# Performance work log

Measured on AMD Instinct MI355X. Metric: run time of the kernel, lower is better.

The kernel has to match this reference:

```python
import jax, jax.numpy as jnp
import numpy as np

B, S, D, H = 64, 512, 512, 512


def setup_inputs() -> dict:
    key = jax.random.key(0)
    ks = jax.random.split(key, 8)
    k = 1.0 / np.sqrt(H)  # torch nn.LSTM init bound
    return {
        "x": jax.random.normal(ks[0], (B, S, D), dtype=jnp.float32),
        "emb": jax.random.normal(ks[1], (B, D), dtype=jnp.float32),
        "h_n": jax.random.normal(ks[2], (1, B, H), dtype=jnp.float32),
        "c_n": jax.random.normal(ks[3], (1, B, H), dtype=jnp.float32),
        "W_ih": jax.random.uniform(ks[4], (4 * H, D), jnp.float32, -k, k),
        "W_hh": jax.random.uniform(ks[5], (4 * H, H), jnp.float32, -k, k),
        "b_ih": jax.random.uniform(ks[6], (4 * H,), jnp.float32, -k, k),
        "b_hh": jax.random.uniform(ks[7], (4 * H,), jnp.float32, -k, k),
    }


def reference(x, emb, h_n, c_n, W_ih, W_hh, b_ih, b_hh):
    # Decoder feeds emb at step 0, then teacher-forces x[:, i-1] at step i.
    inputs = jnp.concatenate([emb[:, None, :], x[:, :-1, :]], axis=1)  # [B,S,D]
    # Precompute input-to-hidden gates for the whole sequence (one big GEMM).
    xg = jnp.einsum("bsd,gd->bsg", inputs, W_ih) + b_ih + b_hh  # [B,S,4H]

    def step(carry, xg_t):
        h, c = carry
        gates = xg_t + h @ W_hh.T  # [B,4H]; torch gate order: i,f,g,o
        i, f, g, o = jnp.split(gates, 4, axis=-1)
        c = jax.nn.sigmoid(f) * c + jax.nn.sigmoid(i) * jnp.tanh(g)
        h = jax.nn.sigmoid(o) * jnp.tanh(c)
        return (h, c), h

    (_, _), ys = jax.lax.scan(step, (h_n[0], c_n[0]), jnp.swapaxes(xg, 0, 1))
    return jnp.swapaxes(ys, 0, 1)  # [B,S,H]
```

## Files before the change

kernel.cpp:

```cpp
#include <hip/hip_runtime.h>
#include <cstdint>


#define SS 512
#define DD 512
#define HH 512

typedef __attribute__((ext_vector_type(8))) short s8;
typedef __attribute__((ext_vector_type(4))) float f4;

__device__ inline short f2bf(float f) {
  unsigned u = __float_as_uint(f);
  u += 0x7fffu + ((u >> 16) & 1u);
  return (short)(u >> 16);
}

__device__ inline s8 cvt8(f4 a, f4 b) {
  s8 v;
  v[0]=f2bf(a[0]); v[1]=f2bf(a[1]); v[2]=f2bf(a[2]); v[3]=f2bf(a[3]);
  v[4]=f2bf(b[0]); v[5]=f2bf(b[1]); v[6]=f2bf(b[2]); v[7]=f2bf(b[3]);
  return v;
}

__device__ inline float sigm(float x)  { return 1.f / (1.f + __expf(-x)); }
__device__ inline float tanh_f(float x){ return 1.f - 2.f / (__expf(2.f*x) + 1.f); }

__device__ inline void stq_agent(void* p, unsigned long long v) {
  __hip_atomic_store((unsigned long long*)p, v, __ATOMIC_RELAXED, __HIP_MEMORY_SCOPE_AGENT);
}
__device__ inline unsigned long long ldq_agent(const void* p) {
  return __hip_atomic_load((const unsigned long long*)p, __ATOMIC_RELAXED, __HIP_MEMORY_SCOPE_AGENT);
}
__device__ inline void st4_agent(unsigned* p, unsigned v) {
  __hip_atomic_store(p, v, __ATOMIC_RELAXED, __HIP_MEMORY_SCOPE_AGENT);
}
__device__ inline unsigned ld4_agent(const unsigned* p) {
  return __hip_atomic_load(p, __ATOMIC_RELAXED, __HIP_MEMORY_SCOPE_AGENT);
}
__device__ inline void drain_vm() {
  asm volatile("s_waitcnt vmcnt(0)" ::: "memory");
}

__device__ inline unsigned flag_ballot(const unsigned* flags, int lane, unsigned target) {
  unsigned v = ld4_agent(flags + (lane & 31));
  unsigned long long b = __ballot(v >= target);
  return (unsigned)b & (unsigned)(b >> 32);
}

__device__ inline void heavy_barrier(unsigned* cnt, unsigned target) {
  drain_vm();
  __syncthreads();
  if (threadIdx.x == 0) {
    __threadfence();
    __hip_atomic_fetch_add(cnt, 1u, __ATOMIC_RELAXED, __HIP_MEMORY_SCOPE_AGENT);
    unsigned guard = 0;
    while (__hip_atomic_load(cnt, __ATOMIC_RELAXED, __HIP_MEMORY_SCOPE_AGENT) < target) {
      __builtin_amdgcn_s_sleep(2);
      if (++guard > 10000000u) break;
    }
  }
  __syncthreads();
  (void)__hip_atomic_load(cnt, __ATOMIC_ACQUIRE, __HIP_MEMORY_SCOPE_AGENT);
  __syncthreads();
}

__launch_bounds__(256, 1)
__global__ void lstm_kernel(const float* __restrict__ x,   const float* __restrict__ emb,
                            const float* __restrict__ h_n, const float* __restrict__ c_n,
                            const float* __restrict__ W_ih, const float* __restrict__ W_hh,
                            const float* __restrict__ b_ih, const float* __restrict__ b_hh,
                            float* __restrict__ out, char* __restrict__ ws)
{
  const int tid  = threadIdx.x;
  const int wave = tid >> 6, lane = tid & 63;
  const int quad = lane >> 4, n = lane & 15;
  const int c  = blockIdx.x & 7;
  const int wg = blockIdx.x >> 3;

  unsigned* cnt   = (unsigned*)(ws + (size_t)c * 128);
  unsigned* flags = (unsigned*)(ws + 1024 + (size_t)c * 128);
  char*     hbuf  = ws + 4096;
  char*     xfrag = ws + 4096 + 2*8*8192;
  char*     xfc   = xfrag + (size_t)c * ((size_t)SS * 8192);

  __shared__ float lout[2][128];

  {
    int widc = wg*4 + wave;
    for (int item = widc; item < 4096; item += 128) {
      int t = item & 511, bl = item >> 9;
      const float* src = (t == 0) ? (emb + (size_t)(c*8 + bl) * DD)
                                  : (x + ((size_t)(c*8 + bl) * SS + (t-1)) * DD);
      f4 f0 = *(const f4*)(src + lane*8);
      f4 f1 = *(const f4*)(src + lane*8 + 4);
      s8 v = cvt8(f0, f1);
      *(s8*)(xfc + (size_t)t*8192 + (lane>>2)*512 + (lane&3)*128 + bl*16) = v;
    }
  }

  s8 wihf[16], whhf[16];
  {
    int r = wave*16 + n;
    int rowg = (r & 3)*512 + wg*16 + (r >> 2);
    const float* pih = W_ih + (size_t)rowg * DD + quad*8;
    const float* phh = W_hh + (size_t)rowg * HH + quad*8;
#pragma unroll
    for (int kk = 0; kk < 16; ++kk) {
      f4 a0 = *(const f4*)(pih + kk*32);
      f4 a1 = *(const f4*)(pih + kk*32 + 4);
      wihf[kk] = cvt8(a0, a1);
      f4 b0 = *(const f4*)(phh + kk*32);
      f4 b1 = *(const f4*)(phh + kk*32 + 4);
      whhf[kk] = cvt8(b0, b1);
    }
  }

  const int u = wg*16 + wave*4 + quad;
  f4 biasv;
  biasv[0] = b_ih[0*512+u] + b_hh[0*512+u];
  biasv[1] = b_ih[1*512+u] + b_hh[1*512+u];
  biasv[2] = b_ih[2*512+u] + b_hh[2*512+u];
  biasv[3] = b_ih[3*512+u] + b_hh[3*512+u];
  float creg = 0.f, h0 = 0.f;
  if (n < 8) {
    creg = c_n[(size_t)(c*8 + n)*HH + u];
    h0   = h_n[(size_t)(c*8 + n)*HH + u];
  }
  const int u0 = wg*16 + wave*4;
  const int hsoff = (u0>>5)*512 + ((u0>>3)&3)*128 + (u0&7)*2;

  {
    int sv = (int)(unsigned short)f2bf(h0);
    int p2 = sv | (__shfl_xor(sv, 16) << 16);
    int p4 = __shfl_xor(p2, 32);
    unsigned long long packed = (unsigned)p2 | ((unsigned long long)(unsigned)p4 << 32);
    if (lane < 8) stq_agent(hbuf + (size_t)c*8192 + hsoff + lane*16, packed);
  }

  heavy_barrier(cnt, 32u);

  const s8 zero8 = {0,0,0,0,0,0,0,0};
  s8 xf[16], hf[16];
#pragma unroll
  for (int kk = 0; kk < 16; ++kk) { xf[kk] = zero8; hf[kk] = zero8; }

  f4 accx = biasv, accx2 = {0.f,0.f,0.f,0.f};
  if (n < 8) {
    const char* xb = xfc + quad*128 + n*16;
#pragma unroll
    for (int kk = 0; kk < 16; ++kk)
      xf[kk] = *(const s8*)(xb + kk*512);
  }
#pragma unroll
  for (int kk = 0; kk < 8; ++kk)
    accx  = __builtin_amdgcn_mfma_f32_16x16x32_bf16(wihf[kk],   xf[kk],   accx,  0,0,0);
#pragma unroll
  for (int kk = 0; kk < 8; ++kk)
    accx2 = __builtin_amdgcn_mfma_f32_16x16x32_bf16(wihf[kk+8], xf[kk+8], accx2, 0,0,0);

  unsigned pm = 0xFFFFu;
  unsigned rdy = 0u;
  if (n < 8) {
    const char* b0 = hbuf + (size_t)c*8192 + quad*128 + n*16;
#pragma unroll
    for (int kk = 0; kk < 16; ++kk) {
      union { unsigned long long qq[2]; s8 v; } tmp;
      tmp.qq[0] = ldq_agent(b0 + kk*512);
      tmp.qq[1] = ldq_agent(b0 + kk*512 + 8);
      hf[kk] = tmp.v;
    }
  }

  float* const outb = out + (size_t)(c*8)*SS*HH + wg*16;

  for (int t = 0; t < SS; ++t) {
    const char* hrd = hbuf + (size_t)(((t  )&1)*8 + c)*8192;
    char*       hwr = hbuf + (size_t)(((t+1)&1)*8 + c)*8192;

    if (pm != 0xFFFFu) {
      unsigned missing = 0u;
#pragma unroll
      for (int kk = 0; kk < 16; ++kk)
        if (!(pm & (1u << kk))) missing |= 3u << (2*kk);
      unsigned guard = 0;
      while ((rdy & missing) != missing) {
        rdy |= flag_ballot(flags, lane, (unsigned)t);
        if (++guard > 4000000u) break;
      }
      asm volatile("" ::: "memory");
      if (n < 8) {
        const char* b0 = hrd + quad*128 + n*16;
#pragma unroll
        for (int kk = 0; kk < 16; ++kk) {
          if (!(pm & (1u << kk))) {
            union { unsigned long long qq[2]; s8 v; } tmp;
            tmp.qq[0] = ldq_agent(b0 + kk*512);
            tmp.qq[1] = ldq_agent(b0 + kk*512 + 8);
            hf[kk] = tmp.v;
          }
        }
      }
    }

    f4 acc = accx, acc2 = accx2;
#pragma unroll
    for (int kk = 0; kk < 8; ++kk)
      acc  = __builtin_amdgcn_mfma_f32_16x16x32_bf16(whhf[kk],   hf[kk],   acc,  0,0,0);
#pragma unroll
    for (int kk = 0; kk < 8; ++kk)
      acc2 = __builtin_amdgcn_mfma_f32_16x16x32_bf16(whhf[kk+8], hf[kk+8], acc2, 0,0,0);
    acc += acc2;

    float iv = sigm(acc[0]);
    float fv = sigm(acc[1]);
    float gv = tanh_f(acc[2]);
    float ov = sigm(acc[3]);
    creg = fv*creg + iv*gv;
    float hv = ov * tanh_f(creg);

    if (n < 8) lout[t&1][n*16 + wave*4 + quad] = hv;

    if (t < SS-1) {
      int sv = (int)(unsigned short)f2bf(hv);
      int p2 = sv | (__shfl_xor(sv, 16) << 16);
      int p4 = __shfl_xor(p2, 32);
      unsigned long long packed = (unsigned)p2 | ((unsigned long long)(unsigned)p4 << 32);
      if (lane < 8) stq_agent(hwr + hsoff + lane*16, packed);
    }

    drain_vm();
    __syncthreads();

    if (t < SS-1 && tid == 0)
      st4_agent(flags + wg, (unsigned)(t + 1));

    if (tid < 128) {
      int n2 = tid >> 4, ul = tid & 15;
      outb[((size_t)n2*SS + t)*HH + ul] = lout[t&1][n2*16 + ul];
    }

    if (t < SS-1) {
      if (n < 8) {
        const char* xb = xfc + (size_t)(t+1)*8192 + quad*128 + n*16;
#pragma unroll
        for (int kk = 0; kk < 16; ++kk)
          xf[kk] = *(const s8*)(xb + kk*512);
      }
      accx = biasv; accx2[0]=0.f; accx2[1]=0.f; accx2[2]=0.f; accx2[3]=0.f;
#pragma unroll
      for (int kk = 0; kk < 8; ++kk)
        accx  = __builtin_amdgcn_mfma_f32_16x16x32_bf16(wihf[kk],   xf[kk],   accx,  0,0,0);
#pragma unroll
      for (int kk = 0; kk < 8; ++kk)
        accx2 = __builtin_amdgcn_mfma_f32_16x16x32_bf16(wihf[kk+8], xf[kk+8], accx2, 0,0,0);

      rdy = flag_ballot(flags, lane, (unsigned)(t + 1));
      asm volatile("" ::: "memory");
      pm = 0u;
#pragma unroll
      for (int kk = 0; kk < 16; ++kk) {
        const unsigned need = 3u << (2*kk);
        if ((rdy & need) == need) {
          if (n < 8) {
            const char* b1 = hwr + quad*128 + n*16;
            union { unsigned long long qq[2]; s8 v; } tmp;
            tmp.qq[0] = ldq_agent(b1 + kk*512);
            tmp.qq[1] = ldq_agent(b1 + kk*512 + 8);
            hf[kk] = tmp.v;
          }
          pm |= 1u << kk;
        }
      }
    }
  }
}

extern "C" void kernel_launch(void* const* d_in, const int* in_sizes, int n_in,
                              void* d_out, int out_size, void* d_ws, size_t ws_size,
                              hipStream_t stream) {
  const float* x    = (const float*)d_in[0];
  const float* emb  = (const float*)d_in[1];
  const float* h_n  = (const float*)d_in[2];
  const float* c_n  = (const float*)d_in[3];
  const float* W_ih = (const float*)d_in[4];
  const float* W_hh = (const float*)d_in[5];
  const float* b_ih = (const float*)d_in[6];
  const float* b_hh = (const float*)d_in[7];

  hipMemsetAsync(d_ws, 0, 2048, stream);

  lstm_kernel<<<dim3(256), dim3(256), 0, stream>>>(
      x, emb, h_n, c_n, W_ih, W_hh, b_ih, b_hh, (float*)d_out, (char*)d_ws);
}
```

Baseline: 1.632 ms.

## Replace per-workgroup flag sync with tagged h-buffer data for inter-block handoff

Each 8-byte chunk of packed h now carries a step tag stored next to it, so consumers check the tags and accept the data directly. This removes the separate flag array, the per-step drain and __syncthreads, and the flag store. The output write also moves from an LDS staging buffer to a shuffle plus a direct vectorized store, which takes the block-wide barrier off the critical path. The cost is a larger h buffer, extra tag loads and a larger memset. Correctness now depends on the ordering of the data store and the tag store, and nothing but compiler barriers enforces that order.

```diff
diff --git a/kernel.cpp b/kernel.cpp
--- a/kernel.cpp
+++ b/kernel.cpp
@@ -31,20 +31,14 @@
 __device__ inline unsigned long long ldq_agent(const void* p) {
   return __hip_atomic_load((const unsigned long long*)p, __ATOMIC_RELAXED, __HIP_MEMORY_SCOPE_AGENT);
 }
-__device__ inline void st4_agent(unsigned* p, unsigned v) {
-  __hip_atomic_store(p, v, __ATOMIC_RELAXED, __HIP_MEMORY_SCOPE_AGENT);
-}
 __device__ inline unsigned ld4_agent(const unsigned* p) {
   return __hip_atomic_load(p, __ATOMIC_RELAXED, __HIP_MEMORY_SCOPE_AGENT);
 }
 __device__ inline void drain_vm() {
   asm volatile("s_waitcnt vmcnt(0)" ::: "memory");
 }
-
-__device__ inline unsigned flag_ballot(const unsigned* flags, int lane, unsigned target) {
-  unsigned v = ld4_agent(flags + (lane & 31));
-  unsigned long long b = __ballot(v >= target);
-  return (unsigned)b & (unsigned)(b >> 32);
+__device__ inline unsigned long long tagpair(unsigned t) {
+  return (unsigned long long)t * 0x0000000100000001ull;
 }
 
 __device__ inline void heavy_barrier(unsigned* cnt, unsigned target) {
@@ -77,13 +71,10 @@
   const int c  = blockIdx.x & 7;
   const int wg = blockIdx.x >> 3;
 
-  unsigned* cnt   = (unsigned*)(ws + (size_t)c * 128);
-  unsigned* flags = (unsigned*)(ws + 1024 + (size_t)c * 128);
-  char*     hbuf  = ws + 4096;
-  char*     xfrag = ws + 4096 + 2*8*8192;
+  unsigned* cnt  = (unsigned*)(ws + (size_t)c * 128);
+  char*     hbuf = ws + 4096;
+  char*     xfrag = ws + 4096 + 2*8*16384;
   char*     xfc   = xfrag + (size_t)c * ((size_t)SS * 8192);
-
-  __shared__ float lout[2][128];
 
   {
     int widc = wg*4 + wave;
@@ -127,14 +118,19 @@
     h0   = h_n[(size_t)(c*8 + n)*HH + u];
   }
   const int u0 = wg*16 + wave*4;
-  const int hsoff = (u0>>5)*512 + ((u0>>3)&3)*128 + (u0&7)*2;
+  const int pslot = (u0 >> 5)*1024 + ((u0 >> 2) & 7)*128;
 
   {
     int sv = (int)(unsigned short)f2bf(h0);
     int p2 = sv | (__shfl_xor(sv, 16) << 16);
     int p4 = __shfl_xor(p2, 32);
     unsigned long long packed = (unsigned)p2 | ((unsigned long long)(unsigned)p4 << 32);
-    if (lane < 8) stq_agent(hbuf + (size_t)c*8192 + hsoff + lane*16, packed);
+    if (lane < 8) {
+      char* s = hbuf + (size_t)c*16384 + pslot + lane*16;
+      stq_agent(s, packed);
+      asm volatile("" ::: "memory");
+      stq_agent(s + 8, tagpair(1u));
+    }
   }
 
   heavy_barrier(cnt, 32u);
@@ -159,46 +155,52 @@
     accx2 = __builtin_amdgcn_mfma_f32_16x16x32_bf16(wihf[kk+8], xf[kk+8], accx2, 0,0,0);
 
   unsigned pm = 0xFFFFu;
-  unsigned rdy = 0u;
   if (n < 8) {
-    const char* b0 = hbuf + (size_t)c*8192 + quad*128 + n*16;
+    const char* cb = hbuf + (size_t)c*16384 + quad*256 + n*16;
 #pragma unroll
     for (int kk = 0; kk < 16; ++kk) {
       union { unsigned long long qq[2]; s8 v; } tmp;
-      tmp.qq[0] = ldq_agent(b0 + kk*512);
-      tmp.qq[1] = ldq_agent(b0 + kk*512 + 8);
+      tmp.qq[0] = ldq_agent(cb + kk*1024);
+      tmp.qq[1] = ldq_agent(cb + kk*1024 + 128);
       hf[kk] = tmp.v;
     }
   }
 
-  float* const outb = out + (size_t)(c*8)*SS*HH + wg*16;
-
   for (int t = 0; t < SS; ++t) {
-    const char* hrd = hbuf + (size_t)(((t  )&1)*8 + c)*8192;
-    char*       hwr = hbuf + (size_t)(((t+1)&1)*8 + c)*8192;
+    const char* hrd = hbuf + (size_t)(((t  )&1)*8 + c)*16384;
+    char*       hwr = hbuf + (size_t)(((t+1)&1)*8 + c)*16384;
+    const unsigned T = (unsigned)t + 1u;
 
     if (pm != 0xFFFFu) {
-      unsigned missing = 0u;
-#pragma unroll
-      for (int kk = 0; kk < 16; ++kk)
-        if (!(pm & (1u << kk))) missing |= 3u << (2*kk);
+      const char* cb = hrd + quad*256 + n*16;
       unsigned guard = 0;
-      while ((rdy & missing) != missing) {
-        rdy |= flag_ballot(flags, lane, (unsigned)t);
-        if (++guard > 4000000u) break;
-      }
-      asm volatile("" ::: "memory");
-      if (n < 8) {
-        const char* b0 = hrd + quad*128 + n*16;
-#pragma unroll
-        for (int kk = 0; kk < 16; ++kk) {
-          if (!(pm & (1u << kk))) {
-            union { unsigned long long qq[2]; s8 v; } tmp;
-            tmp.qq[0] = ldq_agent(b0 + kk*512);
-            tmp.qq[1] = ldq_agent(b0 + kk*512 + 8);
-            hf[kk] = tmp.v;
-          }
+      while (!__all(pm == 0xFFFFu)) {
+        if (n < 8 && pm != 0xFFFFu) {
+          unsigned tA[16], tB[16];
+          unsigned long long dA[16], dB[16];
+#pragma unroll
+          for (int kk = 0; kk < 16; ++kk)
+            if (!(pm & (1u << kk))) {
+              tA[kk] = ld4_agent((const unsigned*)(cb + kk*1024 + 8));
+              tB[kk] = ld4_agent((const unsigned*)(cb + kk*1024 + 136));
+            }
+          asm volatile("" ::: "memory");
+#pragma unroll
+          for (int kk = 0; kk < 16; ++kk)
+            if (!(pm & (1u << kk))) {
+              dA[kk] = ldq_agent(cb + kk*1024);
+              dB[kk] = ldq_agent(cb + kk*1024 + 128);
+            }
+#pragma unroll
+          for (int kk = 0; kk < 16; ++kk)
+            if (!(pm & (1u << kk)) && tA[kk] == T && tB[kk] == T) {
+              union { unsigned long long qq[2]; s8 v; } tmp;
+              tmp.qq[0] = dA[kk]; tmp.qq[1] = dB[kk];
+              hf[kk] = tmp.v;
+              pm |= 1u << kk;
+            }
         }
+        if (++guard > 200000u) break;
       }
     }
 
@@ -218,25 +220,29 @@
     creg = fv*creg + iv*gv;
     float hv = ov * tanh_f(creg);
 
-    if (n < 8) lout[t&1][n*16 + wave*4 + quad] = hv;
-
     if (t < SS-1) {
       int sv = (int)(unsigned short)f2bf(hv);
       int p2 = sv | (__shfl_xor(sv, 16) << 16);
       int p4 = __shfl_xor(p2, 32);
       unsigned long long packed = (unsigned)p2 | ((unsigned long long)(unsigned)p4 << 32);
-      if (lane < 8) stq_agent(hwr + hsoff + lane*16, packed);
-    }
-
-    drain_vm();
-    __syncthreads();
-
-    if (t < SS-1 && tid == 0)
-      st4_agent(flags + wg, (unsigned)(t + 1));
-
-    if (tid < 128) {
-      int n2 = tid >> 4, ul = tid & 15;
-      outb[((size_t)n2*SS + t)*HH + ul] = lout[t&1][n2*16 + ul];
+      if (lane < 8) {
+        char* s = hwr + pslot + lane*16;
+        stq_agent(s, packed);
+        asm volatile("" ::: "memory");
+        stq_agent(s + 8, tagpair((unsigned)t + 2u));
+        asm volatile("" ::: "memory");
+      }
+    }
+
+    {
+      float o0 = __shfl(hv, n);
+      float o1 = __shfl(hv, 16 + n);
+      float o2 = __shfl(hv, 32 + n);
+      float o3 = __shfl(hv, 48 + n);
+      if (quad == 0 && n < 8) {
+        f4 o; o[0]=o0; o[1]=o1; o[2]=o2; o[3]=o3;
+        *(f4*)(out + ((size_t)(c*8 + n)*SS + t)*HH + u0) = o;
+      }
     }
 
     if (t < SS-1) {
@@ -254,22 +260,32 @@
       for (int kk = 0; kk < 8; ++kk)
         accx2 = __builtin_amdgcn_mfma_f32_16x16x32_bf16(wihf[kk+8], xf[kk+8], accx2, 0,0,0);
 
-      rdy = flag_ballot(flags, lane, (unsigned)(t + 1));
-      asm volatile("" ::: "memory");
-      pm = 0u;
-#pragma unroll
-      for (int kk = 0; kk < 16; ++kk) {
-        const unsigned need = 3u << (2*kk);
-        if ((rdy & need) == need) {
-          if (n < 8) {
-            const char* b1 = hwr + quad*128 + n*16;
+      pm = 0xFFFFu;
+      if (n < 8) {
+        pm = 0u;
+        const unsigned T2 = (unsigned)t + 2u;
+        const char* cb = hwr + quad*256 + n*16;
+        unsigned tA[16], tB[16];
+        unsigned long long dA[16], dB[16];
+#pragma unroll
+        for (int kk = 0; kk < 16; ++kk) {
+          tA[kk] = ld4_agent((const unsigned*)(cb + kk*1024 + 8));
+          tB[kk] = ld4_agent((const unsigned*)(cb + kk*1024 + 136));
+        }
+        asm volatile("" ::: "memory");
+#pragma unroll
+        for (int kk = 0; kk < 16; ++kk) {
+          dA[kk] = ldq_agent(cb + kk*1024);
+          dB[kk] = ldq_agent(cb + kk*1024 + 128);
+        }
+#pragma unroll
+        for (int kk = 0; kk < 16; ++kk)
+          if (tA[kk] == T2 && tB[kk] == T2) {
             union { unsigned long long qq[2]; s8 v; } tmp;
-            tmp.qq[0] = ldq_agent(b1 + kk*512);
-            tmp.qq[1] = ldq_agent(b1 + kk*512 + 8);
+            tmp.qq[0] = dA[kk]; tmp.qq[1] = dB[kk];
             hf[kk] = tmp.v;
+            pm |= 1u << kk;
           }
-          pm |= 1u << kk;
-        }
       }
     }
   }
@@ -287,7 +303,7 @@
   const float* b_ih = (const float*)d_in[6];
   const float* b_hh = (const float*)d_in[7];
 
-  hipMemsetAsync(d_ws, 0, 2048, stream);
+  hipMemsetAsync(d_ws, 0, 4096 + 2*8*16384, stream);
 
   lstm_kernel<<<dim3(256), dim3(256), 0, stream>>>(
       x, emb, h_n, c_n, W_ih, W_hh, b_ih, b_hh, (float*)d_out, (char*)d_ws);
```

After: 3.104 ms. 1.9x slower.
